# Optimization experiments

Hardware: AMD Instinct MI355X
Metric: run time of the kernel (lower is better)

The kernel has to match this reference:

```python
import jax, jax.numpy as jnp
import numpy as np

HEADS = 16
D_HEAD = 64
EPS = 1e-5


def _ln(x, g, b):
    m = jnp.mean(x, axis=-1, keepdims=True)
    v = jnp.var(x, axis=-1, keepdims=True)
    return (x - m) * jax.lax.rsqrt(v + EPS) * g + b


def _attn(xq, xc, Wq, Wk, Wv, Wo, bo):
    # Wq: [dim, inner], Wk/Wv: [ctx_dim, inner], Wo: [inner, dim]
    B, N, _ = xq.shape
    S = xc.shape[1]
    q = (xq @ Wq).reshape(B, N, HEADS, D_HEAD)
    k = (xc @ Wk).reshape(B, S, HEADS, D_HEAD)
    v = (xc @ Wv).reshape(B, S, HEADS, D_HEAD)
    scale = D_HEAD ** -0.5
    scores = jnp.einsum('bnhd,bshd->bhns', q, k) * scale
    attn = jax.nn.softmax(scores, axis=-1)
    out = jnp.einsum('bhns,bshd->bnhd', attn, v).reshape(B, N, HEADS * D_HEAD)
    return out @ Wo + bo


def _geglu_ff(x, Wp, bp, Wf, bf):
    h = x @ Wp + bp  # [B,N,2*inner]
    a, gate = jnp.split(h, 2, axis=-1)
    # torch F.gelu default is exact (erf) gelu
    return (a * jax.nn.gelu(gate, approximate=False)) @ Wf + bf


def setup_inputs() -> dict:
    key = jax.random.key(0)
    ks = jax.random.split(key, 16)
    dim, ctx, inner, ffin = 1024, 768, HEADS * D_HEAD, 4 * 1024
    def w(k, i, o):
        return jax.random.normal(k, (i, o), jnp.float32) * (i ** -0.5)
    inp = {
        'x': jax.random.normal(ks[0], (4, 2048, dim), jnp.float32),
        'context': jax.random.normal(ks[1], (4, 77, ctx), jnp.float32),
        'Wq1': w(ks[2], dim, inner), 'Wk1': w(ks[3], dim, inner), 'Wv1': w(ks[4], dim, inner),
        'Wo1': w(ks[5], inner, dim), 'bo1': jnp.zeros((dim,), jnp.float32),
        'Wq2': w(ks[6], dim, inner), 'Wk2': w(ks[7], ctx, inner), 'Wv2': w(ks[8], ctx, inner),
        'Wo2': w(ks[9], inner, dim), 'bo2': jnp.zeros((dim,), jnp.float32),
        'Wp': w(ks[10], dim, 2 * ffin), 'bp': jnp.zeros((2 * ffin,), jnp.float32),
        'Wf': w(ks[11], ffin, dim), 'bf': jnp.zeros((dim,), jnp.float32),
        'g1': jnp.ones((dim,), jnp.float32), 'b1': jnp.zeros((dim,), jnp.float32),
        'g2': jnp.ones((dim,), jnp.float32), 'b2': jnp.zeros((dim,), jnp.float32),
        'g3': jnp.ones((dim,), jnp.float32), 'b3': jnp.zeros((dim,), jnp.float32),
    }
    return inp


def reference(x, context, Wq1, Wk1, Wv1, Wo1, bo1, Wq2, Wk2, Wv2, Wo2, bo2,
              Wp, bp, Wf, bf, g1, b1, g2, b2, g3, b3):
    x = _attn(_ln(x, g1, b1), _ln(x, g1, b1), Wq1, Wk1, Wv1, Wo1, bo1) + x
    x = _attn(_ln(x, g2, b2), context, Wq2, Wk2, Wv2, Wo2, bo2) + x
    x = _geglu_ff(_ln(x, g3, b3), Wp, bp, Wf, bf) + x
    return x
```

## Files before the change

kernel.cpp:

```cpp
#include <hip/hip_runtime.h>

typedef unsigned short u16;
typedef __bf16 bf16x8 __attribute__((ext_vector_type(8)));
typedef float f32x4 __attribute__((ext_vector_type(4)));

#define HEADS 16
#define DHEAD 64
#define DIM 1024
#define NTOK 2048
#define BATCH 4
#define CTXD 768
#define SCROSS 77
#define FFIN 4096

__device__ inline float bf2f(u16 v) { return __uint_as_float(((unsigned)v) << 16); }
__device__ inline u16 f2bf(float f) {
    unsigned u = __float_as_uint(f);
    unsigned r = u + 0x7fffu + ((u >> 16) & 1u);
    return (u16)(r >> 16);
}
__device__ inline f32x4 f4zero() { f32x4 v; v[0]=0.f; v[1]=0.f; v[2]=0.f; v[3]=0.f; return v; }
__device__ inline bf16x8 as_bf16x8(uint4 u) { union { uint4 a; bf16x8 b; } c; c.a = u; return c.b; }

__device__ inline void gload_lds16(const u16* g, u16* l) {
    __builtin_amdgcn_global_load_lds((const __attribute__((address_space(1))) unsigned*)g,
                                     (__attribute__((address_space(3))) unsigned*)l, 16, 0, 0);
}

__global__ __launch_bounds__(256) void wt_k(const float* __restrict__ W, u16* __restrict__ WT,
                                            int K, int N, float scale) {
    __shared__ u16 Ts[64][72];
    int k0 = blockIdx.x * 64, n0 = blockIdx.y * 64;
    int t = threadIdx.x;
    int r = t >> 2, c4 = (t & 3) * 16;
    const float* wp = W + (size_t)(k0 + r) * N + n0 + c4;
    #pragma unroll
    for (int j = 0; j < 4; j++) {
        float4 v = *(const float4*)(wp + j * 4);
        Ts[c4 + j * 4 + 0][r] = f2bf(v.x * scale);
        Ts[c4 + j * 4 + 1][r] = f2bf(v.y * scale);
        Ts[c4 + j * 4 + 2][r] = f2bf(v.z * scale);
        Ts[c4 + j * 4 + 3][r] = f2bf(v.w * scale);
    }
    __syncthreads();
    int n = t >> 2, kc = (t & 3) * 16;
    u16* op = WT + (size_t)(n0 + n) * K + k0 + kc;
    *(uint4*)op       = *(const uint4*)&Ts[n][kc];
    *(uint4*)(op + 8) = *(const uint4*)&Ts[n][kc + 8];
}

__global__ __launch_bounds__(256) void cvt_k(const float* __restrict__ X, u16* __restrict__ Y, int n4) {
    int i = blockIdx.x * 256 + threadIdx.x;
    if (i < n4) {
        float4 v = *(const float4*)(X + (size_t)i * 4);
        uint2 o;
        o.x = (unsigned)f2bf(v.x) | ((unsigned)f2bf(v.y) << 16);
        o.y = (unsigned)f2bf(v.z) | ((unsigned)f2bf(v.w) << 16);
        *(uint2*)(Y + (size_t)i * 4) = o;
    }
}

__global__ __launch_bounds__(256) void ln_k(const float* __restrict__ X, const float* __restrict__ G,
                                            const float* __restrict__ Bt, u16* __restrict__ Y) {
    int row = blockIdx.x;
    int t = threadIdx.x;
    int w = t >> 6, lane = t & 63;
    float4 xv = *(const float4*)(X + (size_t)row * DIM + t * 4);
    float s = xv.x + xv.y + xv.z + xv.w;
    float s2 = xv.x*xv.x + xv.y*xv.y + xv.z*xv.z + xv.w*xv.w;
    for (int off = 1; off < 64; off <<= 1) {
        s  += __shfl_xor(s,  off, 64);
        s2 += __shfl_xor(s2, off, 64);
    }
    __shared__ float rs[4], rs2[4];
    if (lane == 0) { rs[w] = s; rs2[w] = s2; }
    __syncthreads();
    float S_ = rs[0] + rs[1] + rs[2] + rs[3];
    float S2_ = rs2[0] + rs2[1] + rs2[2] + rs2[3];
    float mean = S_ * (1.0f / DIM);
    float var = fmaxf(S2_ * (1.0f / DIM) - mean * mean, 0.f);
    float rstd = rsqrtf(var + 1e-5f);
    int col = t * 4;
    float4 g = *(const float4*)(G + col);
    float4 b = *(const float4*)(Bt + col);
    float y0 = (xv.x - mean) * rstd * g.x + b.x;
    float y1 = (xv.y - mean) * rstd * g.y + b.y;
    float y2 = (xv.z - mean) * rstd * g.z + b.z;
    float y3 = (xv.w - mean) * rstd * g.w + b.w;
    uint2 o;
    o.x = (unsigned)f2bf(y0) | ((unsigned)f2bf(y1) << 16);
    o.y = (unsigned)f2bf(y2) | ((unsigned)f2bf(y3) << 16);
    *(uint2*)(Y + (size_t)row * DIM + col) = o;
}

template<typename TC, bool RESID>
__global__ __launch_bounds__(256) void gemm128(const u16* __restrict__ A, int lda,
                                               const u16* __restrict__ BT,
                                               const float* __restrict__ bias, const float* resid,
                                               TC* C, int ldc, int M, int N, int K) {
    __shared__ __align__(16) u16 As[128 * 32];
    __shared__ __align__(16) u16 Bs[128 * 32];
    int m0 = blockIdx.x * 128, n0 = blockIdx.y * 128;
    int t = threadIdx.x;
    int w = t >> 6, lane = t & 63;
    int quad = lane >> 4, l16 = lane & 15;
    int mh = (w & 1) * 64, nh = (w >> 1) * 64;
    f32x4 acc[4][4];
    #pragma unroll
    for (int i = 0; i < 4; i++)
        #pragma unroll
        for (int j = 0; j < 4; j++) acc[i][j] = f4zero();
    int sr = t >> 2;
    int sc8 = (t & 3) * 8;
    int ra0 = min(m0 + sr, M - 1);
    int ra1 = min(m0 + sr + 64, M - 1);
    const u16* ga0 = A + (size_t)ra0 * lda + sc8;
    const u16* ga1 = A + (size_t)ra1 * lda + sc8;
    const u16* gb0 = BT + (size_t)(n0 + sr) * K + sc8;
    const u16* gb1 = BT + (size_t)(n0 + sr + 64) * K + sc8;
    u16* lA0 = &As[w * 512];
    u16* lA1 = &As[2048 + w * 512];
    u16* lB0 = &Bs[w * 512];
    u16* lB1 = &Bs[2048 + w * 512];
    for (int k0 = 0; k0 < K; k0 += 32) {
        __syncthreads();
        gload_lds16(ga0 + k0, lA0);
        gload_lds16(ga1 + k0, lA1);
        gload_lds16(gb0 + k0, lB0);
        gload_lds16(gb1 + k0, lB1);
        __syncthreads();
        bf16x8 af[4], bfv[4];
        #pragma unroll
        for (int i = 0; i < 4; i++) {
            af[i]  = as_bf16x8(*(const uint4*)&As[(mh + i * 16 + l16) * 32 + quad * 8]);
            bfv[i] = as_bf16x8(*(const uint4*)&Bs[(nh + i * 16 + l16) * 32 + quad * 8]);
        }
        #pragma unroll
        for (int i = 0; i < 4; i++)
            #pragma unroll
            for (int j = 0; j < 4; j++)
                acc[i][j] = __builtin_amdgcn_mfma_f32_16x16x32_bf16(af[i], bfv[j], acc[i][j], 0, 0, 0);
    }
    #pragma unroll
    for (int j = 0; j < 4; j++) {
        int gn = n0 + nh + j * 16 + l16;
        float bv = bias ? bias[gn] : 0.f;
        #pragma unroll
        for (int i = 0; i < 4; i++) {
            #pragma unroll
            for (int r = 0; r < 4; r++) {
                int gm = m0 + mh + i * 16 + quad * 4 + r;
                if (gm < M) {
                    float v = acc[i][j][r] + bv;
                    if constexpr (RESID) v += resid[(size_t)gm * N + gn];
                    if constexpr (__is_same(TC, u16)) C[(size_t)gm * ldc + gn] = f2bf(v);
                    else                              C[(size_t)gm * ldc + gn] = v;
                }
            }
        }
    }
}

__global__ __launch_bounds__(256, 2) void gemm_geglu(const u16* __restrict__ A,
                                                     const u16* __restrict__ BT,
                                                     const float* __restrict__ bp,
                                                     u16* __restrict__ Gb, int M) {
    __shared__ __align__(16) u16 As[128 * 32];
    __shared__ __align__(16) u16 Bs1[128 * 32];
    __shared__ __align__(16) u16 Bs2[128 * 32];
    const int K = DIM;
    int m0 = blockIdx.x * 128, n0 = blockIdx.y * 128;
    int t = threadIdx.x;
    int w = t >> 6, lane = t & 63;
    int quad = lane >> 4, l16 = lane & 15;
    int mh = (w & 1) * 64, nh = (w >> 1) * 64;
    f32x4 acc1[4][4], acc2[4][4];
    #pragma unroll
    for (int i = 0; i < 4; i++)
        #pragma unroll
        for (int j = 0; j < 4; j++) { acc1[i][j] = f4zero(); acc2[i][j] = f4zero(); }
    int sr = t >> 2;
    int sc8 = (t & 3) * 8;
    const u16* ga0 = A + (size_t)(m0 + sr) * K + sc8;
    const u16* ga1 = A + (size_t)(m0 + sr + 64) * K + sc8;
    const u16* gb0 = BT + (size_t)(n0 + sr) * K + sc8;
    const u16* gb1 = BT + (size_t)(n0 + sr + 64) * K + sc8;
    const u16* gc0 = BT + (size_t)(FFIN + n0 + sr) * K + sc8;
    const u16* gc1 = BT + (size_t)(FFIN + n0 + sr + 64) * K + sc8;
    u16* lA0 = &As[w * 512];
    u16* lA1 = &As[2048 + w * 512];
    u16* lB0 = &Bs1[w * 512];
    u16* lB1 = &Bs1[2048 + w * 512];
    u16* lC0 = &Bs2[w * 512];
    u16* lC1 = &Bs2[2048 + w * 512];
    for (int k0 = 0; k0 < K; k0 += 32) {
        __syncthreads();
        gload_lds16(ga0 + k0, lA0);
        gload_lds16(ga1 + k0, lA1);
        gload_lds16(gb0 + k0, lB0);
        gload_lds16(gb1 + k0, lB1);
        gload_lds16(gc0 + k0, lC0);
        gload_lds16(gc1 + k0, lC1);
        __syncthreads();
        bf16x8 af[4];
        #pragma unroll
        for (int i = 0; i < 4; i++)
            af[i] = as_bf16x8(*(const uint4*)&As[(mh + i * 16 + l16) * 32 + quad * 8]);
        #pragma unroll
        for (int j = 0; j < 4; j++) {
            bf16x8 b1 = as_bf16x8(*(const uint4*)&Bs1[(nh + j * 16 + l16) * 32 + quad * 8]);
            bf16x8 b2 = as_bf16x8(*(const uint4*)&Bs2[(nh + j * 16 + l16) * 32 + quad * 8]);
            #pragma unroll
            for (int i = 0; i < 4; i++) {
                acc1[i][j] = __builtin_amdgcn_mfma_f32_16x16x32_bf16(af[i], b1, acc1[i][j], 0, 0, 0);
                acc2[i][j] = __builtin_amdgcn_mfma_f32_16x16x32_bf16(af[i], b2, acc2[i][j], 0, 0, 0);
            }
        }
    }
    #pragma unroll
    for (int j = 0; j < 4; j++) {
        int gn = n0 + nh + j * 16 + l16;
        float b1v = bp[gn];
        float b2v = bp[FFIN + gn];
        #pragma unroll
        for (int i = 0; i < 4; i++) {
            #pragma unroll
            for (int r = 0; r < 4; r++) {
                int gm = m0 + mh + i * 16 + quad * 4 + r;
                float a = acc1[i][j][r] + b1v;
                float g = acc2[i][j][r] + b2v;
                float v = a * (0.5f * g * (1.f + erff(g * 0.70710678118654752f)));
                Gb[(size_t)gm * FFIN + gn] = f2bf(v);
            }
        }
    }
}

__global__ __launch_bounds__(256) void attn_k(const u16* Q, int ldq, const u16* __restrict__ K,
                                              const u16* __restrict__ V, int ldkv,
                                              u16* O, int S) {
    __shared__ __align__(16) u16 Ksh[2][4096];
    __shared__ __align__(16) u16 Vt[4][2048];
    __shared__ __align__(16) u16 Pb[4][4][512];
    int bh = blockIdx.x;
    int b = bh >> 4, h = bh & 15;
    int q0 = blockIdx.y * 64;
    int t = threadIdx.x;
    int w = t >> 6, lane = t & 63;
    int quad = lane >> 4, l16 = lane & 15;
    const u16* Qp = Q + ((size_t)b * NTOK + q0) * ldq + h * DHEAD;
    const u16* Kp = K + (size_t)b * S * ldkv + h * DHEAD;
    const u16* Vp = V + (size_t)b * S * ldkv + h * DHEAD;
    bf16x8 qf[2];
    #pragma unroll
    for (int ds = 0; ds < 2; ds++)
        qf[ds] = as_bf16x8(*(const uint4*)(Qp + (size_t)(w * 16 + l16) * ldq + ds * 32 + quad * 8));
    float l_l = 0.f;
    f32x4 o_acc[4];
    #pragma unroll
    for (int dt = 0; dt < 4; dt++) o_acc[dt] = f4zero();
    int cA = w * 128 + lane;
    int krA = cA >> 2, kdA = (cA & 3) * 8;
    int krB = (cA + 64) >> 2, kdB = ((cA + 64) & 3) * 8;
    int vd = (t >> 5) * 8;
    int vk = (t & 31) * 4;
    int vkk = vk >> 5, vcol = vk & 31;
    int nkt = (S + 127) / 128;
    for (int kt = 0; kt < nkt; kt++) {
        int kbase = kt * 128;
        bool full = (kbase + 128) <= S;
        __syncthreads();
        {
            int rA = min(kbase + krA, S - 1);
            int rB = min(kbase + krB, S - 1);
            const u16* kgA = Kp + (size_t)rA * ldkv;
            const u16* kgB = Kp + (size_t)rB * ldkv;
            gload_lds16(kgA + kdA,      &Ksh[0][w * 1024]);
            gload_lds16(kgB + kdB,      &Ksh[0][w * 1024 + 512]);
            gload_lds16(kgA + 32 + kdA, &Ksh[1][w * 1024]);
            gload_lds16(kgB + 32 + kdB, &Ksh[1][w * 1024 + 512]);
        }
        {
            union { uint4 u; u16 e[8]; } vr[4];
            #pragma unroll
            for (int j = 0; j < 4; j++) {
                int key = min(kbase + vk + j, S - 1);
                vr[j].u = *(const uint4*)(Vp + (size_t)key * ldkv + vd);
            }
            #pragma unroll
            for (int d = 0; d < 8; d++) {
                uint2 p;
                p.x = (unsigned)vr[0].e[d] | ((unsigned)vr[1].e[d] << 16);
                p.y = (unsigned)vr[2].e[d] | ((unsigned)vr[3].e[d] << 16);
                *(uint2*)&Vt[vkk][(vd + d) * 32 + vcol] = p;
            }
        }
        __syncthreads();
        f32x4 sc[8];
        #pragma unroll
        for (int sub = 0; sub < 8; sub++) {
            bf16x8 kf0 = as_bf16x8(*(const uint4*)&Ksh[0][(sub * 16 + l16) * 32 + quad * 8]);
            bf16x8 kf1 = as_bf16x8(*(const uint4*)&Ksh[1][(sub * 16 + l16) * 32 + quad * 8]);
            f32x4 s = __builtin_amdgcn_mfma_f32_16x16x32_bf16(kf0, qf[0], f4zero(), 0, 0, 0);
            sc[sub] = __builtin_amdgcn_mfma_f32_16x16x32_bf16(kf1, qf[1], s, 0, 0, 0);
        }
        if (!full) {
            #pragma unroll
            for (int sub = 0; sub < 8; sub++)
                #pragma unroll
                for (int r = 0; r < 4; r++)
                    if (kbase + sub * 16 + quad * 4 + r >= S) sc[sub][r] = -1e30f;
        }
        float psum = 0.f;
        #pragma unroll
        for (int sub = 0; sub < 8; sub++) {
            float p0 = __builtin_amdgcn_exp2f(sc[sub][0]);
            float p1 = __builtin_amdgcn_exp2f(sc[sub][1]);
            float p2 = __builtin_amdgcn_exp2f(sc[sub][2]);
            float p3 = __builtin_amdgcn_exp2f(sc[sub][3]);
            psum += (p0 + p1) + (p2 + p3);
            uint2 pk;
            pk.x = __builtin_amdgcn_perm(__float_as_uint(p1), __float_as_uint(p0), 0x07060302);
            pk.y = __builtin_amdgcn_perm(__float_as_uint(p3), __float_as_uint(p2), 0x07060302);
            *(uint2*)&Pb[w][sub >> 1][l16 * 32 + (sub & 1) * 16 + quad * 4] = pk;
        }
        l_l += psum;
        #pragma unroll
        for (int kk = 0; kk < 4; kk++) {
            bf16x8 pf = as_bf16x8(*(const uint4*)&Pb[w][kk][l16 * 32 + quad * 8]);
            #pragma unroll
            for (int dt = 0; dt < 4; dt++) {
                bf16x8 vf = as_bf16x8(*(const uint4*)&Vt[kk][(dt * 16 + l16) * 32 + quad * 8]);
                o_acc[dt] = __builtin_amdgcn_mfma_f32_16x16x32_bf16(pf, vf, o_acc[dt], 0, 0, 0);
            }
        }
    }
    float l_tot = l_l;
    l_tot += __shfl_xor(l_tot, 16, 64);
    l_tot += __shfl_xor(l_tot, 32, 64);
    #pragma unroll
    for (int r = 0; r < 4; r++) {
        float lr = __shfl(l_tot, quad * 4 + r, 64);
        float invl = (lr > 0.f) ? (1.f / lr) : 0.f;
        int gq = q0 + w * 16 + quad * 4 + r;
        #pragma unroll
        for (int dt = 0; dt < 4; dt++) {
            O[((size_t)b * NTOK + gq) * ldq + h * DHEAD + dt * 16 + l16] = f2bf(o_acc[dt][r] * invl);
        }
    }
}

extern "C" void kernel_launch(void* const* d_in, const int* in_sizes, int n_in,
                              void* d_out, int out_size, void* d_ws, size_t ws_size,
                              hipStream_t stream) {
    const float* x   = (const float*)d_in[0];
    const float* ctx = (const float*)d_in[1];
    const float* Wq1 = (const float*)d_in[2];
    const float* Wk1 = (const float*)d_in[3];
    const float* Wv1 = (const float*)d_in[4];
    const float* Wo1 = (const float*)d_in[5];
    const float* bo1 = (const float*)d_in[6];
    const float* Wq2 = (const float*)d_in[7];
    const float* Wk2 = (const float*)d_in[8];
    const float* Wv2 = (const float*)d_in[9];
    const float* Wo2 = (const float*)d_in[10];
    const float* bo2 = (const float*)d_in[11];
    const float* Wp  = (const float*)d_in[12];
    const float* bp  = (const float*)d_in[13];
    const float* Wf  = (const float*)d_in[14];
    const float* bfb = (const float*)d_in[15];
    const float* g1  = (const float*)d_in[16];
    const float* b1  = (const float*)d_in[17];
    const float* g2  = (const float*)d_in[18];
    const float* b2  = (const float*)d_in[19];
    const float* g3  = (const float*)d_in[20];
    const float* b3  = (const float*)d_in[21];
    float* out = (float*)d_out;

    const int M = BATCH * NTOK;
    const int Mc = BATCH * SCROSS;
    u16* ws = (u16*)d_ws;
    size_t o = 0;
    u16* WqT1 = ws + o; o += (size_t)DIM * DIM;
    u16* WkT1 = ws + o; o += (size_t)DIM * DIM;
    u16* WvT1 = ws + o; o += (size_t)DIM * DIM;
    u16* WoT1 = ws + o; o += (size_t)DIM * DIM;
    u16* WqT2 = ws + o; o += (size_t)DIM * DIM;
    u16* WoT2 = ws + o; o += (size_t)DIM * DIM;
    u16* WkT2 = ws + o; o += (size_t)DIM * CTXD;
    u16* WvT2 = ws + o; o += (size_t)DIM * CTXD;
    u16* WpT  = ws + o; o += (size_t)(2 * FFIN) * DIM;
    u16* WfT  = ws + o; o += (size_t)DIM * FFIN;
    u16* ctxb = ws + o; o += (size_t)Mc * CTXD;
    u16* KVc  = ws + o; o += (size_t)Mc * 2048;
    u16* P    = ws + o; o += (size_t)M * DIM;
    u16* QKV  = ws + o; o += (size_t)M * 3072;
    u16* reg2 = ws + o; o += (size_t)M * DIM * 2;
    float* X1 = (float*)reg2;
    u16* gb = QKV;

    dim3 blk(256);
    const float qscale = 0.125f * 1.4426950408889634f;

    wt_k<<<dim3(16, 16), blk, 0, stream>>>(Wq1, WqT1, DIM, DIM, qscale);
    wt_k<<<dim3(16, 16), blk, 0, stream>>>(Wk1, WkT1, DIM, DIM, 1.f);
    wt_k<<<dim3(16, 16), blk, 0, stream>>>(Wv1, WvT1, DIM, DIM, 1.f);
    wt_k<<<dim3(16, 16), blk, 0, stream>>>(Wo1, WoT1, DIM, DIM, 1.f);
    wt_k<<<dim3(16, 16), blk, 0, stream>>>(Wq2, WqT2, DIM, DIM, qscale);
    wt_k<<<dim3(16, 16), blk, 0, stream>>>(Wo2, WoT2, DIM, DIM, 1.f);
    wt_k<<<dim3(12, 16), blk, 0, stream>>>(Wk2, WkT2, CTXD, DIM, 1.f);
    wt_k<<<dim3(12, 16), blk, 0, stream>>>(Wv2, WvT2, CTXD, DIM, 1.f);
    wt_k<<<dim3(16, 128), blk, 0, stream>>>(Wp, WpT, DIM, 2 * FFIN, 1.f);
    wt_k<<<dim3(64, 16), blk, 0, stream>>>(Wf, WfT, FFIN, DIM, 1.f);
    cvt_k<<<dim3((Mc * CTXD / 4 + 255) / 256), blk, 0, stream>>>(ctx, ctxb, Mc * CTXD / 4);

    ln_k<<<dim3(M), blk, 0, stream>>>(x, g1, b1, P);
    gemm128<u16, false><<<dim3(M / 128, 3072 / 128), blk, 0, stream>>>(
        P, DIM, WqT1, nullptr, nullptr, QKV, 3072, M, 3072, DIM);
    attn_k<<<dim3(BATCH * HEADS, NTOK / 64), blk, 0, stream>>>(
        QKV, 3072, QKV + 1024, QKV + 2048, 3072, QKV, NTOK);
    gemm128<float, true><<<dim3(M / 128, DIM / 128), blk, 0, stream>>>(
        QKV, 3072, WoT1, bo1, x, X1, DIM, M, DIM, DIM);

    ln_k<<<dim3(M), blk, 0, stream>>>(X1, g2, b2, P);
    gemm128<u16, false><<<dim3(M / 128, DIM / 128), blk, 0, stream>>>(
        P, DIM, WqT2, nullptr, nullptr, QKV, 3072, M, DIM, DIM);
    gemm128<u16, false><<<dim3((Mc + 127) / 128, 2048 / 128), blk, 0, stream>>>(
        ctxb, CTXD, WkT2, nullptr, nullptr, KVc, 2048, Mc, 2048, CTXD);
    attn_k<<<dim3(BATCH * HEADS, NTOK / 64), blk, 0, stream>>>(
        QKV, 3072, KVc, KVc + 1024, 2048, QKV, SCROSS);
    gemm128<float, true><<<dim3(M / 128, DIM / 128), blk, 0, stream>>>(
        QKV, 3072, WoT2, bo2, X1, out, DIM, M, DIM, DIM);

    ln_k<<<dim3(M), blk, 0, stream>>>(out, g3, b3, P);
    gemm_geglu<<<dim3(M / 128, FFIN / 128), blk, 0, stream>>>(P, WpT, bp, gb, M);
    gemm128<float, true><<<dim3(M / 128, DIM / 128), blk, 0, stream>>>(
        gb, FFIN, WfT, bfb, out, out, DIM, M, DIM, FFIN);
}
```

Before: 945.1 us.

## Add 256x256 double-buffered pipelined GEMM for QKV and GEGLU projections

```diff
diff --git a/kernel.cpp b/kernel.cpp
--- a/kernel.cpp
+++ b/kernel.cpp
@@ -28,7 +28,7 @@
 }
 
 __global__ __launch_bounds__(256) void wt_k(const float* __restrict__ W, u16* __restrict__ WT,
-                                            int K, int N, float scale) {
+                                            int K, int N, float scale, int remap) {
     __shared__ u16 Ts[64][72];
     int k0 = blockIdx.x * 64, n0 = blockIdx.y * 64;
     int t = threadIdx.x;
@@ -44,7 +44,9 @@
     }
     __syncthreads();
     int n = t >> 2, kc = (t & 3) * 16;
-    u16* op = WT + (size_t)(n0 + n) * K + k0 + kc;
+    int ng = n0 + n;
+    if (remap) ng = ((ng & 4095) >> 4) * 32 + ((ng >> 12) << 4) + (ng & 15);
+    u16* op = WT + (size_t)ng * K + k0 + kc;
     *(uint4*)op       = *(const uint4*)&Ts[n][kc];
     *(uint4*)(op + 8) = *(const uint4*)&Ts[n][kc + 8];
 }
@@ -161,77 +163,151 @@
     }
 }
 
-__global__ __launch_bounds__(256, 2) void gemm_geglu(const u16* __restrict__ A,
-                                                     const u16* __restrict__ BT,
-                                                     const float* __restrict__ bp,
-                                                     u16* __restrict__ Gb, int M) {
-    __shared__ __align__(16) u16 As[128 * 32];
-    __shared__ __align__(16) u16 Bs1[128 * 32];
-    __shared__ __align__(16) u16 Bs2[128 * 32];
-    const int K = DIM;
-    int m0 = blockIdx.x * 128, n0 = blockIdx.y * 128;
+
+#define BAR() __builtin_amdgcn_s_barrier()
+#define SB0() __builtin_amdgcn_sched_barrier(0)
+#define PRIO1() __builtin_amdgcn_s_setprio(1)
+#define PRIO0() __builtin_amdgcn_s_setprio(0)
+#define WAIT_VM6() asm volatile("s_waitcnt vmcnt(6)" ::: "memory")
+#define WAIT_VM0() asm volatile("s_waitcnt vmcnt(0)" ::: "memory")
+#define WAIT_LGKM0() asm volatile("s_waitcnt lgkmcnt(0)" ::: "memory")
+#define WAIT_LGKM8() asm volatile("s_waitcnt lgkmcnt(8)" ::: "memory")
+
+#define STAGE_A_R(P, h, q, TAU) gload_lds16(gA + (size_t)((h) * 128 + (q) * 64) * 1024 + (TAU) * 64, \
+                                            lA + (P) * 16384 + (h) * 8192 + (q) * 4096)
+#define STAGE_B_R(P, h, q, TAU) gload_lds16(gB + (size_t)((h) * 128 + (q) * 64) * 1024 + (TAU) * 64, \
+                                            lB + (P) * 16384 + (h) * 8192 + (q) * 4096)
+#define RD_A(P, fi, ks) as_bf16x8(*(const uint4*)(rdA + (P) * 32768 + (fi) * 2048 + ((ks) ? o1 : o0)))
+#define RD_B(P, fj, ks) as_bf16x8(*(const uint4*)(rdB + (P) * 32768 + (fj) * 2048 + ((ks) ? o1 : o0)))
+#define MM(ai, aj, av, bv) acc[ai][aj] = __builtin_amdgcn_mfma_f32_16x16x32_bf16(av, bv, acc[ai][aj], 0, 0, 0)
+
+#define TILE256(P, S0, S1, T, LAST) do {                                              \
+    if (LAST) { WAIT_VM0(); } else { WAIT_VM6(); }                                    \
+    BAR(); SB0();                                                                     \
+                               \
+    Ar[0][0] = RD_A(P, 0, 0); Ar[0][1] = RD_A(P, 0, 1);                               \
+    Ar[1][0] = RD_A(P, 1, 0); Ar[1][1] = RD_A(P, 1, 1);                               \
+    Ar[2][0] = RD_A(P, 2, 0); Ar[2][1] = RD_A(P, 2, 1);                               \
+    Ar[3][0] = RD_A(P, 3, 0); Ar[3][1] = RD_A(P, 3, 1);                               \
+    Br[0][0] = RD_B(P, 0, 0); Br[0][1] = RD_B(P, 0, 1);                               \
+    Br[1][0] = RD_B(P, 1, 0); Br[1][1] = RD_B(P, 1, 1);                               \
+    if (S0) { STAGE_B_R((P) ^ 1, 1, 0, (T) + 1); STAGE_B_R((P) ^ 1, 1, 1, (T) + 1); } \
+    WAIT_LGKM8();                                                                     \
+    BAR(); WAIT_LGKM0(); SB0(); PRIO1();                                              \
+    MM(0,0,Ar[0][0],Br[0][0]); MM(1,0,Ar[1][0],Br[0][0]); MM(2,0,Ar[2][0],Br[0][0]); MM(3,0,Ar[3][0],Br[0][0]); \
+    MM(0,1,Ar[0][0],Br[1][0]); MM(1,1,Ar[1][0],Br[1][0]); MM(2,1,Ar[2][0],Br[1][0]); MM(3,1,Ar[3][0],Br[1][0]); \
+    MM(0,0,Ar[0][1],Br[0][1]); MM(1,0,Ar[1][1],Br[0][1]); MM(2,0,Ar[2][1],Br[0][1]); MM(3,0,Ar[3][1],Br[0][1]); \
+    MM(0,1,Ar[0][1],Br[1][1]); MM(1,1,Ar[1][1],Br[1][1]); MM(2,1,Ar[2][1],Br[1][1]); MM(3,1,Ar[3][1],Br[1][1]); \
+    PRIO0(); SB0(); BAR();                                                            \
+                                                   \
+    Br[0][0] = RD_B(P, 2, 0); Br[0][1] = RD_B(P, 2, 1);                               \
+    Br[1][0] = RD_B(P, 3, 0); Br[1][1] = RD_B(P, 3, 1);                               \
+    if (S1) { STAGE_A_R(P, 0, 0, (T) + 2); STAGE_A_R(P, 1, 0, (T) + 2); }             \
+    BAR(); WAIT_LGKM0(); SB0(); PRIO1();                                              \
+    MM(0,2,Ar[0][0],Br[0][0]); MM(1,2,Ar[1][0],Br[0][0]); MM(2,2,Ar[2][0],Br[0][0]); MM(3,2,Ar[3][0],Br[0][0]); \
+    MM(0,3,Ar[0][0],Br[1][0]); MM(1,3,Ar[1][0],Br[1][0]); MM(2,3,Ar[2][0],Br[1][0]); MM(3,3,Ar[3][0],Br[1][0]); \
+    MM(0,2,Ar[0][1],Br[0][1]); MM(1,2,Ar[1][1],Br[0][1]); MM(2,2,Ar[2][1],Br[0][1]); MM(3,2,Ar[3][1],Br[0][1]); \
+    MM(0,3,Ar[0][1],Br[1][1]); MM(1,3,Ar[1][1],Br[1][1]); MM(2,3,Ar[2][1],Br[1][1]); MM(3,3,Ar[3][1],Br[1][1]); \
+    PRIO0(); SB0(); BAR();                                                            \
+                                                  \
+    Ar[0][0] = RD_A(P, 4, 0); Ar[0][1] = RD_A(P, 4, 1);                               \
+    Ar[1][0] = RD_A(P, 5, 0); Ar[1][1] = RD_A(P, 5, 1);                               \
+    Ar[2][0] = RD_A(P, 6, 0); Ar[2][1] = RD_A(P, 6, 1);                               \
+    Ar[3][0] = RD_A(P, 7, 0); Ar[3][1] = RD_A(P, 7, 1);                               \
+    if (S1) { STAGE_A_R(P, 0, 1, (T) + 2); STAGE_A_R(P, 1, 1, (T) + 2); }             \
+    BAR(); WAIT_LGKM0(); SB0(); PRIO1();                                              \
+    MM(4,2,Ar[0][0],Br[0][0]); MM(5,2,Ar[1][0],Br[0][0]); MM(6,2,Ar[2][0],Br[0][0]); MM(7,2,Ar[3][0],Br[0][0]); \
+    MM(4,3,Ar[0][0],Br[1][0]); MM(5,3,Ar[1][0],Br[1][0]); MM(6,3,Ar[2][0],Br[1][0]); MM(7,3,Ar[3][0],Br[1][0]); \
+    MM(4,2,Ar[0][1],Br[0][1]); MM(5,2,Ar[1][1],Br[0][1]); MM(6,2,Ar[2][1],Br[0][1]); MM(7,2,Ar[3][1],Br[0][1]); \
+    MM(4,3,Ar[0][1],Br[1][1]); MM(5,3,Ar[1][1],Br[1][1]); MM(6,3,Ar[2][1],Br[1][1]); MM(7,3,Ar[3][1],Br[1][1]); \
+    PRIO0(); SB0(); BAR();                                                            \
+                                              \
+    Br[0][0] = RD_B(P, 0, 0); Br[0][1] = RD_B(P, 0, 1);                               \
+    Br[1][0] = RD_B(P, 1, 0); Br[1][1] = RD_B(P, 1, 1);                               \
+    if (S1) { STAGE_B_R(P, 0, 0, (T) + 2); STAGE_B_R(P, 0, 1, (T) + 2); }             \
+    BAR(); WAIT_LGKM0(); SB0(); PRIO1();                                              \
+    MM(4,0,Ar[0][0],Br[0][0]); MM(5,0,Ar[1][0],Br[0][0]); MM(6,0,Ar[2][0],Br[0][0]); MM(7,0,Ar[3][0],Br[0][0]); \
+    MM(4,1,Ar[0][0],Br[1][0]); MM(5,1,Ar[1][0],Br[1][0]); MM(6,1,Ar[2][0],Br[1][0]); MM(7,1,Ar[3][0],Br[1][0]); \
+    MM(4,0,Ar[0][1],Br[0][1]); MM(5,0,Ar[1][1],Br[0][1]); MM(6,0,Ar[2][1],Br[0][1]); MM(7,0,Ar[3][1],Br[0][1]); \
+    MM(4,1,Ar[0][1],Br[1][1]); MM(5,1,Ar[1][1],Br[1][1]); MM(6,1,Ar[2][1],Br[1][1]); MM(7,1,Ar[3][1],Br[1][1]); \
+    PRIO0(); SB0();                                                                   \
+} while (0)
+
+template<int NBY, int LDC, int EPI>
+__global__ __launch_bounds__(512, 2) void gemm256(const u16* __restrict__ A,
+                                                  const u16* __restrict__ BT,
+                                                  const float* __restrict__ bias,
+                                                  u16* __restrict__ C) {
+    __shared__ __align__(16) u16 As[2][16384];
+    __shared__ __align__(16) u16 Bs[2][16384];
     int t = threadIdx.x;
     int w = t >> 6, lane = t & 63;
     int quad = lane >> 4, l16 = lane & 15;
-    int mh = (w & 1) * 64, nh = (w >> 1) * 64;
-    f32x4 acc1[4][4], acc2[4][4];
-    #pragma unroll
-    for (int i = 0; i < 4; i++)
-        #pragma unroll
-        for (int j = 0; j < 4; j++) { acc1[i][j] = f4zero(); acc2[i][j] = f4zero(); }
-    int sr = t >> 2;
-    int sc8 = (t & 3) * 8;
-    const u16* ga0 = A + (size_t)(m0 + sr) * K + sc8;
-    const u16* ga1 = A + (size_t)(m0 + sr + 64) * K + sc8;
-    const u16* gb0 = BT + (size_t)(n0 + sr) * K + sc8;
-    const u16* gb1 = BT + (size_t)(n0 + sr + 64) * K + sc8;
-    const u16* gc0 = BT + (size_t)(FFIN + n0 + sr) * K + sc8;
-    const u16* gc1 = BT + (size_t)(FFIN + n0 + sr + 64) * K + sc8;
-    u16* lA0 = &As[w * 512];
-    u16* lA1 = &As[2048 + w * 512];
-    u16* lB0 = &Bs1[w * 512];
-    u16* lB1 = &Bs1[2048 + w * 512];
-    u16* lC0 = &Bs2[w * 512];
-    u16* lC1 = &Bs2[2048 + w * 512];
-    for (int k0 = 0; k0 < K; k0 += 32) {
-        __syncthreads();
-        gload_lds16(ga0 + k0, lA0);
-        gload_lds16(ga1 + k0, lA1);
-        gload_lds16(gb0 + k0, lB0);
-        gload_lds16(gb1 + k0, lB1);
-        gload_lds16(gc0 + k0, lC0);
-        gload_lds16(gc1 + k0, lC1);
-        __syncthreads();
-        bf16x8 af[4];
-        #pragma unroll
-        for (int i = 0; i < 4; i++)
-            af[i] = as_bf16x8(*(const uint4*)&As[(mh + i * 16 + l16) * 32 + quad * 8]);
-        #pragma unroll
-        for (int j = 0; j < 4; j++) {
-            bf16x8 b1 = as_bf16x8(*(const uint4*)&Bs1[(nh + j * 16 + l16) * 32 + quad * 8]);
-            bf16x8 b2 = as_bf16x8(*(const uint4*)&Bs2[(nh + j * 16 + l16) * 32 + quad * 8]);
-            #pragma unroll
-            for (int i = 0; i < 4; i++) {
-                acc1[i][j] = __builtin_amdgcn_mfma_f32_16x16x32_bf16(af[i], b1, acc1[i][j], 0, 0, 0);
-                acc2[i][j] = __builtin_amdgcn_mfma_f32_16x16x32_bf16(af[i], b2, acc2[i][j], 0, 0, 0);
-            }
-        }
-    }
-    #pragma unroll
-    for (int j = 0; j < 4; j++) {
-        int gn = n0 + nh + j * 16 + l16;
-        float b1v = bp[gn];
-        float b2v = bp[FFIN + gn];
-        #pragma unroll
-        for (int i = 0; i < 4; i++) {
-            #pragma unroll
-            for (int r = 0; r < 4; r++) {
-                int gm = m0 + mh + i * 16 + quad * 4 + r;
-                float a = acc1[i][j][r] + b1v;
-                float g = acc2[i][j][r] + b2v;
-                float v = a * (0.5f * g * (1.f + erff(g * 0.70710678118654752f)));
-                Gb[(size_t)gm * FFIN + gn] = f2bf(v);
-            }
+    int wm = w >> 2, wn = w & 3;
+    int bid = blockIdx.x;
+    int cpx = (int)gridDim.x >> 3;
+    int swz = (bid & 7) * cpx + (bid >> 3);
+    int bx = swz / NBY, by = swz % NBY;
+    int m0 = bx << 8, n0 = by << 8;
+
+    int ar = t >> 3;
+    int ac = (((t & 7) ^ (ar & 7)) << 3);
+    const u16* gA = A + (size_t)(m0 + ar) * 1024 + ac;
+    const u16* gB = BT + (size_t)(n0 + ar) * 1024 + ac;
+    u16* lA = &As[0][0] + (w << 9);
+    u16* lB = &Bs[0][0] + (w << 9);
+    const char* rdA = (const char*)&As[0][0] + (((wm << 7) + l16) << 7);
+    const char* rdB = (const char*)&Bs[0][0] + (((wn << 6) + l16) << 7);
+    int o0 = (quad << 4) ^ ((l16 & 7) << 4);
+    int o1 = o0 ^ 64;
+
+    f32x4 acc[8][4];
+    #pragma unroll
+    for (int i = 0; i < 8; i++)
+        #pragma unroll
+        for (int j = 0; j < 4; j++) acc[i][j] = f4zero();
+
+    STAGE_A_R(0, 0, 0, 0); STAGE_A_R(0, 0, 1, 0); STAGE_A_R(0, 1, 0, 0); STAGE_A_R(0, 1, 1, 0);
+    STAGE_B_R(0, 0, 0, 0); STAGE_B_R(0, 0, 1, 0); STAGE_B_R(0, 1, 0, 0); STAGE_B_R(0, 1, 1, 0);
+    STAGE_A_R(1, 0, 0, 1); STAGE_A_R(1, 0, 1, 1); STAGE_A_R(1, 1, 0, 1); STAGE_A_R(1, 1, 1, 1);
+    STAGE_B_R(1, 0, 0, 1); STAGE_B_R(1, 0, 1, 1);
+
+    bf16x8 Ar[4][2], Br[2][2];
+    #pragma unroll 1
+    for (int tt = 0; tt < 14; tt += 2) {
+        TILE256(0, 1, 1, tt, 0);
+        TILE256(1, 1, 1, tt + 1, 0);
+    }
+    TILE256(0, 1, 0, 14, 0);
+    TILE256(1, 0, 0, 15, 1);
+
+    if constexpr (EPI == 0) {
+        int gm0 = m0 + wm * 128 + quad * 4;
+        int gn0 = n0 + wn * 64 + l16;
+        #pragma unroll
+        for (int fi = 0; fi < 8; fi++)
+            #pragma unroll
+            for (int fj = 0; fj < 4; fj++)
+                #pragma unroll
+                for (int r = 0; r < 4; r++)
+                    C[(size_t)(gm0 + fi * 16 + r) * LDC + gn0 + fj * 16] = f2bf(acc[fi][fj][r]);
+    } else {
+        int gm0 = m0 + wm * 128 + quad * 4;
+        int oc0 = (n0 >> 1) + wn * 32 + l16;
+        #pragma unroll
+        for (int jp = 0; jp < 2; jp++) {
+            int oc = oc0 + jp * 16;
+            float ba = bias[oc];
+            float bg = bias[FFIN + oc];
+            #pragma unroll
+            for (int fi = 0; fi < 8; fi++)
+                #pragma unroll
+                for (int r = 0; r < 4; r++) {
+                    float a = acc[fi][2 * jp][r] + ba;
+                    float g = acc[fi][2 * jp + 1][r] + bg;
+                    float v = a * (0.5f * g * (1.f + erff(g * 0.70710678118654752f)));
+                    C[(size_t)(gm0 + fi * 16 + r) * LDC + oc] = f2bf(v);
+                }
         }
     }
 }
@@ -402,21 +478,20 @@
     dim3 blk(256);
     const float qscale = 0.125f * 1.4426950408889634f;
 
-    wt_k<<<dim3(16, 16), blk, 0, stream>>>(Wq1, WqT1, DIM, DIM, qscale);
-    wt_k<<<dim3(16, 16), blk, 0, stream>>>(Wk1, WkT1, DIM, DIM, 1.f);
-    wt_k<<<dim3(16, 16), blk, 0, stream>>>(Wv1, WvT1, DIM, DIM, 1.f);
-    wt_k<<<dim3(16, 16), blk, 0, stream>>>(Wo1, WoT1, DIM, DIM, 1.f);
-    wt_k<<<dim3(16, 16), blk, 0, stream>>>(Wq2, WqT2, DIM, DIM, qscale);
-    wt_k<<<dim3(16, 16), blk, 0, stream>>>(Wo2, WoT2, DIM, DIM, 1.f);
-    wt_k<<<dim3(12, 16), blk, 0, stream>>>(Wk2, WkT2, CTXD, DIM, 1.f);
-    wt_k<<<dim3(12, 16), blk, 0, stream>>>(Wv2, WvT2, CTXD, DIM, 1.f);
-    wt_k<<<dim3(16, 128), blk, 0, stream>>>(Wp, WpT, DIM, 2 * FFIN, 1.f);
-    wt_k<<<dim3(64, 16), blk, 0, stream>>>(Wf, WfT, FFIN, DIM, 1.f);
+    wt_k<<<dim3(16, 16), blk, 0, stream>>>(Wq1, WqT1, DIM, DIM, qscale, 0);
+    wt_k<<<dim3(16, 16), blk, 0, stream>>>(Wk1, WkT1, DIM, DIM, 1.f, 0);
+    wt_k<<<dim3(16, 16), blk, 0, stream>>>(Wv1, WvT1, DIM, DIM, 1.f, 0);
+    wt_k<<<dim3(16, 16), blk, 0, stream>>>(Wo1, WoT1, DIM, DIM, 1.f, 0);
+    wt_k<<<dim3(16, 16), blk, 0, stream>>>(Wq2, WqT2, DIM, DIM, qscale, 0);
+    wt_k<<<dim3(16, 16), blk, 0, stream>>>(Wo2, WoT2, DIM, DIM, 1.f, 0);
+    wt_k<<<dim3(12, 16), blk, 0, stream>>>(Wk2, WkT2, CTXD, DIM, 1.f, 0);
+    wt_k<<<dim3(12, 16), blk, 0, stream>>>(Wv2, WvT2, CTXD, DIM, 1.f, 0);
+    wt_k<<<dim3(16, 128), blk, 0, stream>>>(Wp, WpT, DIM, 2 * FFIN, 1.f, 1);
+    wt_k<<<dim3(64, 16), blk, 0, stream>>>(Wf, WfT, FFIN, DIM, 1.f, 0);
     cvt_k<<<dim3((Mc * CTXD / 4 + 255) / 256), blk, 0, stream>>>(ctx, ctxb, Mc * CTXD / 4);
 
     ln_k<<<dim3(M), blk, 0, stream>>>(x, g1, b1, P);
-    gemm128<u16, false><<<dim3(M / 128, 3072 / 128), blk, 0, stream>>>(
-        P, DIM, WqT1, nullptr, nullptr, QKV, 3072, M, 3072, DIM);
+    gemm256<12, 3072, 0><<<dim3(32 * 12), dim3(512), 0, stream>>>(P, WqT1, nullptr, QKV);
     attn_k<<<dim3(BATCH * HEADS, NTOK / 64), blk, 0, stream>>>(
         QKV, 3072, QKV + 1024, QKV + 2048, 3072, QKV, NTOK);
     gemm128<float, true><<<dim3(M / 128, DIM / 128), blk, 0, stream>>>(
@@ -433,7 +508,7 @@
         QKV, 3072, WoT2, bo2, X1, out, DIM, M, DIM, DIM);
 
     ln_k<<<dim3(M), blk, 0, stream>>>(out, g3, b3, P);
-    gemm_geglu<<<dim3(M / 128, FFIN / 128), blk, 0, stream>>>(P, WpT, bp, gb, M);
+    gemm256<32, 4096, 1><<<dim3(32 * 32), dim3(512), 0, stream>>>(P, WpT, bp, gb);
     gemm128<float, true><<<dim3(M / 128, DIM / 128), blk, 0, stream>>>(
         gb, FFIN, WfT, bfb, out, out, DIM, M, DIM, FFIN);
 }
```

After: 949.6 us. About the same (+0.5%).
